# Kernel optimization log

Hardware: AMD Instinct MI355X
Metric: run time of the kernel (lower is better)

The kernel has to match this reference:

```python
import jax, jax.numpy as jnp
import numpy as np

B, N, E, D, H = 1, 100000, 3200000, 16, 128
EPS = 1e-5


def _layer_norm(x, g, b):
    m = jnp.mean(x, axis=-1, keepdims=True)
    v = jnp.mean((x - m) ** 2, axis=-1, keepdims=True)
    return (x - m) * jax.lax.rsqrt(v + EPS) * g + b


def setup_inputs() -> dict:
    key = jax.random.key(0)
    ks = jax.random.split(key, 12)
    inp = {
        "nodes": jax.random.normal(ks[0], (B, N, D), dtype=jnp.float32),
        "edges": jax.random.randint(ks[1], (B, E, 2), 0, N, dtype=jnp.int32),
        "edge_weights": jax.random.uniform(ks[2], (B, E), dtype=jnp.float32),
    }
    dims = [(3 * D, H), (H, H), (H, H), (H, D)]
    for i, (din, dout) in enumerate(dims, start=1):
        inp[f"W{i}"] = jax.random.normal(ks[2 + i], (din, dout), dtype=jnp.float32) * (1.0 / np.sqrt(din))
        inp[f"b{i}"] = jnp.zeros((dout,), dtype=jnp.float32)
        inp[f"g{i}"] = jnp.ones((dout,), dtype=jnp.float32)
        inp[f"be{i}"] = jnp.zeros((dout,), dtype=jnp.float32)
    return inp


def reference(nodes, edges, edge_weights,
              W1, b1, g1, be1, W2, b2, g2, be2,
              W3, b3, g3, be3, W4, b4, g4, be4):
    src = edges[..., 0]  # [B,E]
    dst = edges[..., 1]
    w = edge_weights[..., None]  # [B,E,1]
    # edge-weighted endpoint features
    msg_in = jnp.take_along_axis(nodes, src[..., None], axis=1) * w   # [B,E,D]
    msg_out = jnp.take_along_axis(nodes, dst[..., None], axis=1) * w  # [B,E,D]
    # per-node sum aggregation (scatter-add over edge lists)
    b_idx = jnp.arange(B)[:, None]
    agg_in = jnp.zeros_like(nodes).at[b_idx, dst].add(msg_in)   # in-edges of node i
    agg_out = jnp.zeros_like(nodes).at[b_idx, src].add(msg_out)  # out-edges of node i
    x = jnp.concatenate([agg_in, agg_out, nodes], axis=2)  # [B,N,3D]
    x = jnp.tanh(_layer_norm(x @ W1 + b1, g1, be1))
    x = jnp.tanh(_layer_norm(x @ W2 + b2, g2, be2))
    x = jnp.tanh(_layer_norm(x @ W3 + b3, g3, be3))
    x = jnp.tanh(_layer_norm(x @ W4 + b4, g4, be4))
    return x
```

## Files before the change

kernel.cpp:

```cpp
#include <hip/hip_runtime.h>
#include <stdint.h>

#define DIM 16
#define HID 128
#define TN  64
#define ROWF 132
#define EPSF 1e-5f

typedef unsigned int u32;

#define FIX_SCALE 32768.0f
#define FIX_INV   (1.0f/32768.0f)
#define FIX_BIAS  (1 << 19)
#define FIX_MASK  0x7FFFFFF

__device__ __forceinline__ unsigned long long pack_term(float a, float b) {
    int ia = __float2int_rn(a * FIX_SCALE) + FIX_BIAS;
    int ib = __float2int_rn(b * FIX_SCALE) + FIX_BIAS;
    return (unsigned long long)(unsigned)ia
         | ((unsigned long long)(unsigned)ib << 27)
         | (1ULL << 54);
}

__device__ __forceinline__ float2 unpack_agg(unsigned long long v) {
    int cnt  = (int)(v >> 54);
    int f0   = (int)(v & FIX_MASK);
    int f1   = (int)((v >> 27) & FIX_MASK);
    int base = cnt << 19;
    return make_float2((float)(f0 - base) * FIX_INV,
                       (float)(f1 - base) * FIX_INV);
}

__device__ __forceinline__ float safe_tanh(float x) {
    float a = fabsf(x);
    float e = __expf(2.0f * a);
    float t = 1.0f - 2.0f / (e + 1.0f);
    return copysignf(t, x);
}

__global__ void __launch_bounds__(256) scatter_in_kernel(
    const float* __restrict__ nodes, const int* __restrict__ edges,
    const float* __restrict__ ew,
    unsigned long long* __restrict__ agg_in, int nEdges)
{
    int gid = blockIdx.x * 256 + threadIdx.x;
    int e = gid >> 3;
    if (e >= nEdges) return;
    int p = gid & 7;
    int src = edges[2 * e];
    int dst = edges[2 * e + 1];
    float w  = ew[e];
    float2 vs = *(const float2*)(nodes + src * DIM + 2 * p);
    atomicAdd(&agg_in[(size_t)dst * 8 + p], pack_term(vs.x * w, vs.y * w));
}

__global__ void __launch_bounds__(256) scatter_out_kernel(
    const float* __restrict__ nodes, const int* __restrict__ edges,
    const float* __restrict__ ew,
    unsigned long long* __restrict__ agg_out, int nEdges)
{
    int gid = blockIdx.x * 256 + threadIdx.x;
    int e = gid >> 3;
    if (e >= nEdges) return;
    int p = gid & 7;
    int src = edges[2 * e];
    int dst = edges[2 * e + 1];
    float w  = ew[e];
    float2 vd = *(const float2*)(nodes + dst * DIM + 2 * p);
    atomicAdd(&agg_out[(size_t)src * 8 + p], pack_term(vd.x * w, vd.y * w));
}

template<int K>
__device__ __forceinline__ void dense_ln_tanh(
    const float* __restrict__ W, const float* __restrict__ bias,
    const float* __restrict__ g, const float* __restrict__ be,
    float (&X)[TN][ROWF], int tid)
{
    const int c0 = (tid & 31) * 4;
    const int n0 = (tid >> 5) * 8;
    float acc[8][4];
    {
        float4 bv = *(const float4*)(bias + c0);
        #pragma unroll
        for (int i = 0; i < 8; ++i) {
            acc[i][0] = bv.x; acc[i][1] = bv.y; acc[i][2] = bv.z; acc[i][3] = bv.w;
        }
    }

    float4 w[4];
    #pragma unroll
    for (int kk = 0; kk < 4; ++kk)
        w[kk] = *(const float4*)(W + kk * HID + c0);

    for (int k = 0; k < K; k += 4) {
        float4 wn[4];
        if (k + 4 < K) {
            #pragma unroll
            for (int kk = 0; kk < 4; ++kk)
                wn[kk] = *(const float4*)(W + (k + 4 + kk) * HID + c0);
        }
        #pragma unroll
        for (int i = 0; i < 8; ++i) {
            float4 x = *(const float4*)&X[n0 + i][k];
            float xr[4] = {x.x, x.y, x.z, x.w};
            #pragma unroll
            for (int kk = 0; kk < 4; ++kk) {
                acc[i][0] += xr[kk] * w[kk].x;
                acc[i][1] += xr[kk] * w[kk].y;
                acc[i][2] += xr[kk] * w[kk].z;
                acc[i][3] += xr[kk] * w[kk].w;
            }
        }
        if (k + 4 < K) {
            #pragma unroll
            for (int kk = 0; kk < 4; ++kk) w[kk] = wn[kk];
        }
    }

    float s[8], q[8];
    #pragma unroll
    for (int i = 0; i < 8; ++i) {
        s[i] = acc[i][0] + acc[i][1] + acc[i][2] + acc[i][3];
        q[i] = acc[i][0]*acc[i][0] + acc[i][1]*acc[i][1]
             + acc[i][2]*acc[i][2] + acc[i][3]*acc[i][3];
    }
    #pragma unroll
    for (int m = 1; m <= 16; m <<= 1) {
        #pragma unroll
        for (int i = 0; i < 8; ++i) {
            s[i] += __shfl_xor(s[i], m);
            q[i] += __shfl_xor(q[i], m);
        }
    }

    float4 gv  = *(const float4*)(g + c0);
    float4 bev = *(const float4*)(be + c0);
    float gr[4]  = {gv.x, gv.y, gv.z, gv.w};
    float ber[4] = {bev.x, bev.y, bev.z, bev.w};

    __syncthreads();
    #pragma unroll
    for (int i = 0; i < 8; ++i) {
        float mean = s[i] * (1.0f / HID);
        float var  = fmaxf(q[i] * (1.0f / HID) - mean * mean, 0.0f);
        float r = rsqrtf(var + EPSF);
        float o[4];
        #pragma unroll
        for (int j = 0; j < 4; ++j)
            o[j] = safe_tanh((acc[i][j] - mean) * r * gr[j] + ber[j]);
        *(float4*)&X[n0 + i][c0] = make_float4(o[0], o[1], o[2], o[3]);
    }
    __syncthreads();
}

__global__ void __launch_bounds__(256, 3) mlp_kernel(
    const unsigned long long* __restrict__ agg_in,
    const unsigned long long* __restrict__ agg_out,
    const float* __restrict__ nodes,
    const float* __restrict__ W1, const float* __restrict__ b1, const float* __restrict__ g1, const float* __restrict__ be1,
    const float* __restrict__ W2, const float* __restrict__ b2, const float* __restrict__ g2, const float* __restrict__ be2,
    const float* __restrict__ W3, const float* __restrict__ b3, const float* __restrict__ g3, const float* __restrict__ be3,
    const float* __restrict__ W4, const float* __restrict__ b4, const float* __restrict__ g4, const float* __restrict__ be4,
    float* __restrict__ out, int nNodes)
{
    __shared__ float X[TN][ROWF];

    const int tid = threadIdx.x;
    const int node0 = blockIdx.x * TN;

    for (int i = tid; i < TN * 16; i += 256) {
        int n = i >> 4, f = i & 15;
        int gn = node0 + n;
        float2 v = make_float2(0.f, 0.f);
        if (gn < nNodes) {
            unsigned long long pv = (f < 8)
                ? agg_in [(size_t)gn * 8 + f]
                : agg_out[(size_t)gn * 8 + (f - 8)];
            v = unpack_agg(pv);
        }
        *(float2*)&X[n][2 * f] = v;
    }
    for (int i = tid; i < TN * 4; i += 256) {
        int n = i >> 2, q = i & 3;
        int gn = node0 + n;
        float4 v = make_float4(0.f, 0.f, 0.f, 0.f);
        if (gn < nNodes) v = *(const float4*)(nodes + (size_t)gn * DIM + q * 4);
        *(float4*)&X[n][32 + q * 4] = v;
    }
    __syncthreads();

    dense_ln_tanh<48>(W1, b1, g1, be1, X, tid);
    dense_ln_tanh<128>(W2, b2, g2, be2, X, tid);
    dense_ln_tanh<128>(W3, b3, g3, be3, X, tid);

    {
        const int c2 = tid & 15;
        const int nb = tid >> 4;
        float a[4];
        {
            float bv = b4[c2];
            #pragma unroll
            for (int t = 0; t < 4; ++t) a[t] = bv;
        }
        #pragma unroll 2
        for (int k = 0; k < HID; k += 4) {
            float w[4];
            #pragma unroll
            for (int kk = 0; kk < 4; ++kk) w[kk] = W4[(k + kk) * DIM + c2];
            #pragma unroll
            for (int t = 0; t < 4; ++t) {
                float4 x = *(const float4*)&X[nb + 16 * t][k];
                a[t] += x.x * w[0] + x.y * w[1] + x.z * w[2] + x.w * w[3];
            }
        }
        float s[4], q[4];
        #pragma unroll
        for (int t = 0; t < 4; ++t) { s[t] = a[t]; q[t] = a[t] * a[t]; }
        #pragma unroll
        for (int m = 1; m <= 8; m <<= 1) {
            #pragma unroll
            for (int t = 0; t < 4; ++t) {
                s[t] += __shfl_xor(s[t], m);
                q[t] += __shfl_xor(q[t], m);
            }
        }
        float g4v = g4[c2], be4v = be4[c2];
        #pragma unroll
        for (int t = 0; t < 4; ++t) {
            int node = node0 + nb + 16 * t;
            if (node < nNodes) {
                float mean = s[t] * (1.0f / DIM);
                float var  = fmaxf(q[t] * (1.0f / DIM) - mean * mean, 0.0f);
                float o = safe_tanh((a[t] - mean) * rsqrtf(var + EPSF) * g4v + be4v);
                out[(size_t)node * DIM + c2] = o;
            }
        }
    }
}

extern "C" void kernel_launch(void* const* d_in, const int* in_sizes, int n_in,
                              void* d_out, int out_size, void* d_ws, size_t ws_size,
                              hipStream_t stream)
{
    const float* nodes = (const float*)d_in[0];
    const int*   edges = (const int*)d_in[1];
    const float* ew    = (const float*)d_in[2];
    const float *W1 = (const float*)d_in[3],  *b1 = (const float*)d_in[4],
                *g1 = (const float*)d_in[5],  *be1 = (const float*)d_in[6];
    const float *W2 = (const float*)d_in[7],  *b2 = (const float*)d_in[8],
                *g2 = (const float*)d_in[9],  *be2 = (const float*)d_in[10];
    const float *W3 = (const float*)d_in[11], *b3 = (const float*)d_in[12],
                *g3 = (const float*)d_in[13], *be3 = (const float*)d_in[14];
    const float *W4 = (const float*)d_in[15], *b4 = (const float*)d_in[16],
                *g4 = (const float*)d_in[17], *be4 = (const float*)d_in[18];

    const int N = in_sizes[0] / DIM;
    const int E = in_sizes[2];

    unsigned long long* agg_in  = (unsigned long long*)d_ws;
    unsigned long long* agg_out = agg_in + (size_t)N * 8;

    hipMemsetAsync(d_ws, 0, (size_t)2 * N * 8 * sizeof(unsigned long long), stream);

    long long ethreads = (long long)E * 8;
    int egrid = (int)((ethreads + 255) / 256);
    scatter_in_kernel <<<egrid, 256, 0, stream>>>(nodes, edges, ew, agg_in,  E);
    scatter_out_kernel<<<egrid, 256, 0, stream>>>(nodes, edges, ew, agg_out, E);

    int mgrid = (N + TN - 1) / TN;
    mlp_kernel<<<mgrid, 256, 0, stream>>>(agg_in, agg_out, nodes,
        W1, b1, g1, be1, W2, b2, g2, be2, W3, b3, g3, be3, W4, b4, g4, be4,
        (float*)d_out, N);
}
```

Baseline: 557.6 us.

## Fuse in/out edge scatters into one kernel and make MLP grid persistent

Merges the two edge scatter kernels into a single kernel, so edges, weights and thread indexing are read once and both atomics are issued per thread. The MLP kernel becomes a grid-stride persistent kernel capped at 1024 blocks, with a per-tile device function and a trailing barrier so the shared tile buffer can be reused. This removes one launch and one full pass over the edge list. The costs are twice the atomic traffic per thread and possibly less latency hiding in the MLP when fewer blocks are resident.

```diff
diff --git a/kernel.cpp b/kernel.cpp
--- a/kernel.cpp
+++ b/kernel.cpp
@@ -38,10 +38,11 @@
     return copysignf(t, x);
 }
 
-__global__ void __launch_bounds__(256) scatter_in_kernel(
+__global__ void __launch_bounds__(256) edge_scatter_kernel(
     const float* __restrict__ nodes, const int* __restrict__ edges,
     const float* __restrict__ ew,
-    unsigned long long* __restrict__ agg_in, int nEdges)
+    unsigned long long* __restrict__ agg_in,
+    unsigned long long* __restrict__ agg_out, int nEdges)
 {
     int gid = blockIdx.x * 256 + threadIdx.x;
     int e = gid >> 3;
@@ -51,22 +52,8 @@
     int dst = edges[2 * e + 1];
     float w  = ew[e];
     float2 vs = *(const float2*)(nodes + src * DIM + 2 * p);
-    atomicAdd(&agg_in[(size_t)dst * 8 + p], pack_term(vs.x * w, vs.y * w));
-}
-
-__global__ void __launch_bounds__(256) scatter_out_kernel(
-    const float* __restrict__ nodes, const int* __restrict__ edges,
-    const float* __restrict__ ew,
-    unsigned long long* __restrict__ agg_out, int nEdges)
-{
-    int gid = blockIdx.x * 256 + threadIdx.x;
-    int e = gid >> 3;
-    if (e >= nEdges) return;
-    int p = gid & 7;
-    int src = edges[2 * e];
-    int dst = edges[2 * e + 1];
-    float w  = ew[e];
     float2 vd = *(const float2*)(nodes + dst * DIM + 2 * p);
+    atomicAdd(&agg_in [(size_t)dst * 8 + p], pack_term(vs.x * w, vs.y * w));
     atomicAdd(&agg_out[(size_t)src * 8 + p], pack_term(vd.x * w, vd.y * w));
 }
 
@@ -153,7 +140,7 @@
     __syncthreads();
 }
 
-__global__ void __launch_bounds__(256, 3) mlp_kernel(
+__device__ __forceinline__ void mlp_tile(
     const unsigned long long* __restrict__ agg_in,
     const unsigned long long* __restrict__ agg_out,
     const float* __restrict__ nodes,
@@ -161,13 +148,9 @@
     const float* __restrict__ W2, const float* __restrict__ b2, const float* __restrict__ g2, const float* __restrict__ be2,
     const float* __restrict__ W3, const float* __restrict__ b3, const float* __restrict__ g3, const float* __restrict__ be3,
     const float* __restrict__ W4, const float* __restrict__ b4, const float* __restrict__ g4, const float* __restrict__ be4,
-    float* __restrict__ out, int nNodes)
-{
-    __shared__ float X[TN][ROWF];
-
-    const int tid = threadIdx.x;
-    const int node0 = blockIdx.x * TN;
-
+    float* __restrict__ out, int nNodes, int node0,
+    float (&X)[TN][ROWF], int tid)
+{
     for (int i = tid; i < TN * 16; i += 256) {
         int n = i >> 4, f = i & 15;
         int gn = node0 + n;
@@ -235,6 +218,29 @@
                 out[(size_t)node * DIM + c2] = o;
             }
         }
+    }
+    __syncthreads();
+}
+
+#define MLP_GRID 1024
+
+__global__ void __launch_bounds__(256, 3) mlp_kernel(
+    const unsigned long long* __restrict__ agg_in,
+    const unsigned long long* __restrict__ agg_out,
+    const float* __restrict__ nodes,
+    const float* __restrict__ W1, const float* __restrict__ b1, const float* __restrict__ g1, const float* __restrict__ be1,
+    const float* __restrict__ W2, const float* __restrict__ b2, const float* __restrict__ g2, const float* __restrict__ be2,
+    const float* __restrict__ W3, const float* __restrict__ b3, const float* __restrict__ g3, const float* __restrict__ be3,
+    const float* __restrict__ W4, const float* __restrict__ b4, const float* __restrict__ g4, const float* __restrict__ be4,
+    float* __restrict__ out, int nNodes, int nTiles)
+{
+    __shared__ float X[TN][ROWF];
+    const int tid = threadIdx.x;
+    for (int t = blockIdx.x; t < nTiles; t += MLP_GRID) {
+        mlp_tile(agg_in, agg_out, nodes,
+                 W1, b1, g1, be1, W2, b2, g2, be2,
+                 W3, b3, g3, be3, W4, b4, g4, be4,
+                 out, nNodes, t * TN, X, tid);
     }
 }
 
@@ -264,11 +270,12 @@
 
     long long ethreads = (long long)E * 8;
     int egrid = (int)((ethreads + 255) / 256);
-    scatter_in_kernel <<<egrid, 256, 0, stream>>>(nodes, edges, ew, agg_in,  E);
-    scatter_out_kernel<<<egrid, 256, 0, stream>>>(nodes, edges, ew, agg_out, E);
-
-    int mgrid = (N + TN - 1) / TN;
+    edge_scatter_kernel<<<egrid, 256, 0, stream>>>(nodes, edges, ew,
+                                                   agg_in, agg_out, E);
+
+    int nTiles = (N + TN - 1) / TN;
+    int mgrid = nTiles < MLP_GRID ? nTiles : MLP_GRID;
     mlp_kernel<<<mgrid, 256, 0, stream>>>(agg_in, agg_out, nodes,
         W1, b1, g1, be1, W2, b2, g2, be2, W3, b3, g3, be3, W4, b4, g4, be4,
-        (float*)d_out, N);
-}
+        (float*)d_out, N, nTiles);
+}
```

Measured after the change: 640.1 us. 1.15x slower.
